# Kernel tuning notes

Hardware: AMD Instinct MI355X
Metric: run time of the kernel (lower is better)

The kernel has to match this reference:

```python
import jax, jax.numpy as jnp
import numpy as np

N_EMBD = 1024
HEAD_SIZE = 64
B, T = 8, 4096


def setup_inputs() -> dict:
    key = jax.random.key(0)
    kx, kk, kq, kv = jax.random.split(key, 4)
    scale = 1.0 / np.sqrt(N_EMBD)
    x = jax.random.normal(kx, (B, T, N_EMBD), dtype=jnp.float32)
    # nn.Linear(N_EMBD, head_size, bias=False) weights, stored as [in, out] for x @ W
    W_k = jax.random.uniform(kk, (N_EMBD, HEAD_SIZE), dtype=jnp.float32, minval=-scale, maxval=scale)
    W_q = jax.random.uniform(kq, (N_EMBD, HEAD_SIZE), dtype=jnp.float32, minval=-scale, maxval=scale)
    W_v = jax.random.uniform(kv, (N_EMBD, HEAD_SIZE), dtype=jnp.float32, minval=-scale, maxval=scale)
    return {"x": x, "W_k": W_k, "W_q": W_q, "W_v": W_v}


def reference(x, W_k, W_q, W_v) -> jnp.ndarray:
    # x: [B,T,E]; projections to [B,T,H]
    k = jnp.einsum("bte,eh->bth", x, W_k)
    q = jnp.einsum("bte,eh->bth", x, W_q)
    v = jnp.einsum("bte,eh->bth", x, W_v)
    H = W_k.shape[1]
    scores = jnp.einsum("bth,bsh->bts", q, k) * (H ** -0.5)  # [B,T,T]
    Tlen = x.shape[1]
    causal = jnp.tril(jnp.ones((Tlen, Tlen), dtype=bool))
    scores = jnp.where(causal, scores, -jnp.inf)
    attn = jax.nn.softmax(scores, axis=-1)
    # dropout is identity in eval mode (deterministic reference)
    return jnp.einsum("bts,bsh->bth", attn, v)
```

## Files before the change

### kernel.cpp

```cpp
#include <hip/hip_runtime.h>
#include <hip/hip_bf16.h>


#define BB 8
#define TT 4096
#define EE 1024
#define HH 64

typedef __attribute__((ext_vector_type(8))) short short8;
typedef __attribute__((ext_vector_type(4))) float floatx4;
typedef short8 __attribute__((may_alias)) short8_a;
typedef uint2 __attribute__((may_alias)) uint2_a;
typedef uint4 __attribute__((may_alias)) uint4_a;
typedef float4 __attribute__((may_alias)) float4_a;

#define GLDS(gp, lp)                                                     \
  __builtin_amdgcn_global_load_lds(                                      \
      (const __attribute__((address_space(1))) unsigned int*)(gp),       \
      (__attribute__((address_space(3))) unsigned int*)(lp), 16, 0, 0)

__device__ __forceinline__ unsigned short f2bf(float f) {
  union { float f; unsigned int u; } v; v.f = f;
  unsigned int r = v.u + 0x7fffu + ((v.u >> 16) & 1u);
  return (unsigned short)(r >> 16);
}
__device__ __forceinline__ unsigned int pk2(float a, float b) {
  return (unsigned int)f2bf(a) | ((unsigned int)f2bf(b) << 16);
}
__device__ __forceinline__ floatx4 fzero() {
  floatx4 z = {0.f, 0.f, 0.f, 0.f};
  return z;
}
__device__ __forceinline__ floatx4 mfma_bf16(short8 a, short8 b, floatx4 c) {
  return __builtin_amdgcn_mfma_f32_16x16x32_bf16(a, b, c, 0, 0, 0);
}
__device__ __forceinline__ short8 pack8(float4 a, float4 b) {
  union { unsigned int u[4]; short8 s; } r;
  r.u[0] = pk2(a.x, a.y);
  r.u[1] = pk2(a.z, a.w);
  r.u[2] = pk2(b.x, b.y);
  r.u[3] = pk2(b.z, b.w);
  return r.s;
}

__global__ __launch_bounds__(256) void wt_kernel(
    const float* __restrict__ Wk, const float* __restrict__ Wq,
    const float* __restrict__ Wv, unsigned short* __restrict__ wt3) {
  __shared__ float tile[64][65];
  const int m = blockIdx.y;
  const int eb = blockIdx.x;
  const float* W = (m == 0) ? Wk : ((m == 1) ? Wq : Wv);
  const int t = threadIdx.x;
  {
    const int r = t >> 2;
    const int c0 = (t & 3) * 16;
    const float* src = W + (size_t)(eb * 64 + r) * 64 + c0;
#pragma unroll
    for (int i = 0; i < 16; ++i) tile[r][c0 + i] = src[i];
  }
  __syncthreads();
  {
    const int h = t >> 2;
    const int e0 = (t & 3) * 16;
    unsigned int w[8];
#pragma unroll
    for (int i = 0; i < 8; ++i)
      w[i] = pk2(tile[e0 + 2 * i][h], tile[e0 + 2 * i + 1][h]);
    unsigned short* dst = wt3 + (size_t)(m * 64 + h) * EE + eb * 64 + e0;
    ((uint4_a*)dst)[0] = make_uint4(w[0], w[1], w[2], w[3]);
    ((uint4_a*)(dst + 8))[0] = make_uint4(w[4], w[5], w[6], w[7]);
  }
}

__global__ __launch_bounds__(256) void proj_kernel(
    const float* __restrict__ x, const unsigned short* __restrict__ wt3,
    unsigned short* __restrict__ kws, unsigned short* __restrict__ qws,
    unsigned short* __restrict__ vtws) {
  __shared__ unsigned short Bl[2][24][512];
  const int t = threadIdx.x;
  const int wv = t >> 6, lane = t & 63;
  const int l16 = lane & 15, quad = lane >> 4;
  const int mshalf = wv & 1;
  const int jbase = (wv >> 1) * 6;
  const size_t row0 = (size_t)blockIdx.x * 64;

  floatx4 acc[6][2];
#pragma unroll
  for (int j = 0; j < 6; ++j)
#pragma unroll
    for (int m2 = 0; m2 < 2; ++m2) acc[j][m2] = fzero();

  const float* xbase = x + (row0 + mshalf * 32 + l16) * EE + quad * 8;

  float4 ra[2][2][2], rb[2][2][2];
#pragma unroll
  for (int m2 = 0; m2 < 2; ++m2)
#pragma unroll
    for (int f = 0; f < 2; ++f)
#pragma unroll
      for (int g = 0; g < 2; ++g)
        ra[m2][f][g] = *(const float4_a*)(xbase + (size_t)m2 * 16 * EE + f * 32 + g * 4);

#define STAGE_B(buf, kc)                                                       \
  {                                                                            \
    _Pragma("unroll") for (int i = 0; i < 6; ++i) {                            \
      const int idx = wv * 6 + i;                                              \
      const int j = idx >> 1, f = idx & 1;                                     \
      const unsigned short* gp =                                               \
          wt3 + (size_t)(j * 16 + l16) * EE + (kc) + f * 32 + quad * 8;        \
      GLDS(gp, &Bl[buf][idx][0]);                                              \
    }                                                                          \
  }

  STAGE_B(0, 0);
  __syncthreads();

  for (int c = 0; c < 16; ++c) {
    const int cur = c & 1;
    if (c < 15) {
      STAGE_B(cur ^ 1, (c + 1) * 64);
#pragma unroll
      for (int m2 = 0; m2 < 2; ++m2)
#pragma unroll
        for (int f = 0; f < 2; ++f)
#pragma unroll
          for (int g = 0; g < 2; ++g)
            rb[m2][f][g] = *(const float4_a*)(xbase + (size_t)m2 * 16 * EE +
                                              (c + 1) * 64 + f * 32 + g * 4);
    }
    short8 af[2][2];
#pragma unroll
    for (int m2 = 0; m2 < 2; ++m2)
#pragma unroll
      for (int f = 0; f < 2; ++f) af[m2][f] = pack8(ra[m2][f][0], ra[m2][f][1]);
#pragma unroll
    for (int j = 0; j < 6; ++j)
#pragma unroll
      for (int f = 0; f < 2; ++f) {
        short8 bf = *(const short8_a*)&Bl[cur][(jbase + j) * 2 + f][lane * 8];
#pragma unroll
        for (int m2 = 0; m2 < 2; ++m2)
          acc[j][m2] = mfma_bf16(af[m2][f], bf, acc[j][m2]);
      }
#pragma unroll
    for (int m2 = 0; m2 < 2; ++m2)
#pragma unroll
      for (int f = 0; f < 2; ++f)
#pragma unroll
        for (int g = 0; g < 2; ++g) ra[m2][f][g] = rb[m2][f][g];
    __syncthreads();
  }
#undef STAGE_B

  const int b = (int)(row0 >> 12);
  const int tt0 = (int)(row0 & (TT - 1));
#pragma unroll
  for (int j = 0; j < 6; ++j) {
    const int jg = jbase + j;
    const int m = jg >> 2;
    const int h0 = (jg & 3) * 16;
#pragma unroll
    for (int m2 = 0; m2 < 2; ++m2) {
      floatx4 a = acc[j][m2];
      const int rbase = mshalf * 32 + m2 * 16 + quad * 4;
      if (m == 0) {
#pragma unroll
        for (int r = 0; r < 4; ++r)
          kws[(row0 + rbase + r) * HH + h0 + l16] = f2bf(a[r]);
      } else if (m == 1) {
#pragma unroll
        for (int r = 0; r < 4; ++r)
          qws[(row0 + rbase + r) * HH + h0 + l16] = f2bf(a[r] * 0.125f);
      } else {
        uint2 p;
        p.x = pk2(a[0], a[1]);
        p.y = pk2(a[2], a[3]);
        ((uint2_a*)&vtws[(size_t)(b * 64 + h0 + l16) * TT + tt0 + rbase])[0] = p;
      }
    }
  }
}

__global__ __launch_bounds__(256) void attn_kernel(
    const unsigned short* __restrict__ kws, const unsigned short* __restrict__ qws,
    const unsigned short* __restrict__ vtws, float* __restrict__ out) {
  __shared__ unsigned short KV[2][16][512];
  __shared__ unsigned short pb[4][16][72];
  const int t = threadIdx.x;
  const int wv = t >> 6, lane = t & 63;
  const int l16 = lane & 15, quad = lane >> 4;
  const int id = (int)blockIdx.x;
  const int r255 = id & 255;
  const int b = r255 & 7;
  const int m = r255 >> 3;
  const int jq = (id < 256) ? m : 63 - m;
  const int q0 = jq * 64;
  const int dt = jq;
  const int qrow = q0 + wv * 16 + l16;

  const unsigned short* qp = qws + ((size_t)b * TT + qrow) * HH + quad * 8;
  short8 qa0 = *(const short8_a*)(qp);
  short8 qa1 = *(const short8_a*)(qp + 32);

  floatx4 o[4];
#pragma unroll
  for (int nt = 0; nt < 4; ++nt) o[nt] = fzero();
  float lsum = 0.f;

#define STAGE_KV(buf, ks)                                                      \
  {                                                                            \
    _Pragma("unroll") for (int i = 0; i < 4; ++i) {                            \
      const int idx = wv * 4 + i;                                              \
      const unsigned short* gp;                                                \
      if (idx < 8) {                                                           \
        const int nt = idx >> 1, f = idx & 1;                                  \
        gp = kws + ((size_t)b * TT + (ks) + nt * 16 + l16) * HH + f * 32 +     \
             quad * 8;                                                         \
      } else {                                                                 \
        const int nt = (idx - 8) >> 1, f = idx & 1;                            \
        gp = vtws + ((size_t)(b * 64 + nt * 16 + l16)) * TT + (ks) + f * 32 +  \
             quad * 8;                                                         \
      }                                                                        \
      GLDS(gp, &KV[buf][idx][0]);                                              \
    }                                                                          \
  }

  STAGE_KV(0, 0);
  __syncthreads();

  for (int kt = 0; kt <= dt; ++kt) {
    const int cur = kt & 1;
    const int ks = kt * 64;
    if (kt < dt) STAGE_KV(cur ^ 1, ks + 64);

    floatx4 s[4];
#pragma unroll
    for (int nt = 0; nt < 4; ++nt) {
      short8 kf0 = *(const short8_a*)&KV[cur][nt * 2][lane * 8];
      short8 kf1 = *(const short8_a*)&KV[cur][nt * 2 + 1][lane * 8];
      floatx4 z = fzero();
      z = mfma_bf16(kf0, qa0, z);
      z = mfma_bf16(kf1, qa1, z);
      s[nt] = z;
    }
    if (kt == dt) {
#pragma unroll
      for (int nt = 0; nt < 4; ++nt)
#pragma unroll
        for (int r = 0; r < 4; ++r) {
          const int key = ks + nt * 16 + quad * 4 + r;
          if (key > qrow) s[nt][r] = -1e30f;
        }
    }
#pragma unroll
    for (int nt = 0; nt < 4; ++nt) {
      const float p0 = __expf(s[nt][0]);
      const float p1 = __expf(s[nt][1]);
      const float p2 = __expf(s[nt][2]);
      const float p3 = __expf(s[nt][3]);
      lsum += (p0 + p1) + (p2 + p3);
      uint2 pw;
      pw.x = pk2(p0, p1);
      pw.y = pk2(p2, p3);
      ((uint2_a*)&pb[wv][l16][nt * 16 + quad * 4])[0] = pw;
    }
    short8 pf0 = *(const short8_a*)&pb[wv][l16][quad * 8];
    short8 pf1 = *(const short8_a*)&pb[wv][l16][quad * 8 + 32];
#pragma unroll
    for (int nt = 0; nt < 4; ++nt) {
      short8 vf0 = *(const short8_a*)&KV[cur][8 + nt * 2][lane * 8];
      short8 vf1 = *(const short8_a*)&KV[cur][8 + nt * 2 + 1][lane * 8];
      o[nt] = mfma_bf16(vf0, pf0, o[nt]);
      o[nt] = mfma_bf16(vf1, pf1, o[nt]);
    }
    __syncthreads();
  }
#undef STAGE_KV

  float lr = lsum;
  lr += __shfl_xor(lr, 16);
  lr += __shfl_xor(lr, 32);
  const float inv = 1.0f / lr;
#pragma unroll
  for (int nt = 0; nt < 4; ++nt) {
    float4 st;
    st.x = o[nt][0] * inv;
    st.y = o[nt][1] * inv;
    st.z = o[nt][2] * inv;
    st.w = o[nt][3] * inv;
    *(float4_a*)&out[((size_t)b * TT + qrow) * HH + nt * 16 + quad * 4] = st;
  }
}

extern "C" void kernel_launch(void* const* d_in, const int* in_sizes, int n_in,
                              void* d_out, int out_size, void* d_ws, size_t ws_size,
                              hipStream_t stream) {
  const float* x = (const float*)d_in[0];
  const float* Wk = (const float*)d_in[1];
  const float* Wq = (const float*)d_in[2];
  const float* Wv = (const float*)d_in[3];
  float* out = (float*)d_out;

  unsigned short* kws = (unsigned short*)d_ws;
  unsigned short* qws = kws + (size_t)BB * TT * HH;
  unsigned short* vtws = qws + (size_t)BB * TT * HH;
  unsigned short* wt3 = vtws + (size_t)BB * TT * HH;

  hipLaunchKernelGGL(wt_kernel, dim3(16, 3), dim3(256), 0, stream, Wk, Wq, Wv, wt3);
  hipLaunchKernelGGL(proj_kernel, dim3(512), dim3(256), 0, stream, x, wt3, kws, qws,
                     vtws);
  hipLaunchKernelGGL(attn_kernel, dim3(512), dim3(256), 0, stream, kws, qws,
                     vtws, out);
}
```

Baseline: 305.0 us.

## Split long causal query tiles across key ranges with a separate combine kernel

Query tiles are split along the key dimension into 1 to 4 chunks depending on their causal length, giving 1280 blocks of roughly even work. Each block writes unnormalised partial outputs and row sums to a workspace, and a new combine kernel adds them and normalises. Two smaller changes ride along: the exponential switches to exp2 with log2(e) folded into the Q scale, and bf16 packing uses the hardware v_cvt_pk_bf16_f32 instruction. The cost is an extra launch plus partial-result traffic through global memory, and the split path is used only when the workspace is large enough.

```diff
diff --git a/kernel.cpp b/kernel.cpp
--- a/kernel.cpp
+++ b/kernel.cpp
@@ -1,11 +1,14 @@
 #include <hip/hip_runtime.h>
 #include <hip/hip_bf16.h>
+#include <math.h>
 
 
 #define BB 8
 #define TT 4096
 #define EE 1024
 #define HH 64
+#define NSLOT 160
+#define SLOTF 4160
 
 typedef __attribute__((ext_vector_type(8))) short short8;
 typedef __attribute__((ext_vector_type(4))) float floatx4;
@@ -25,7 +28,9 @@
   return (unsigned short)(r >> 16);
 }
 __device__ __forceinline__ unsigned int pk2(float a, float b) {
-  return (unsigned int)f2bf(a) | ((unsigned int)f2bf(b) << 16);
+  unsigned int r;
+  asm("v_cvt_pk_bf16_f32 %0, %1, %2" : "=v"(r) : "v"(a), "v"(b));
+  return r;
 }
 __device__ __forceinline__ floatx4 fzero() {
   floatx4 z = {0.f, 0.f, 0.f, 0.f};
@@ -170,7 +175,7 @@
       } else if (m == 1) {
 #pragma unroll
         for (int r = 0; r < 4; ++r)
-          qws[(row0 + rbase + r) * HH + h0 + l16] = f2bf(a[r] * 0.125f);
+          qws[(row0 + rbase + r) * HH + h0 + l16] = f2bf(a[r] * 0.18033688011112042f);
       } else {
         uint2 p;
         p.x = pk2(a[0], a[1]);
@@ -181,21 +186,42 @@
   }
 }
 
+template <bool SPLIT>
 __global__ __launch_bounds__(256) void attn_kernel(
     const unsigned short* __restrict__ kws, const unsigned short* __restrict__ qws,
-    const unsigned short* __restrict__ vtws, float* __restrict__ out) {
+    const unsigned short* __restrict__ vtws, float* __restrict__ dst) {
   __shared__ unsigned short KV[2][16][512];
   __shared__ unsigned short pb[4][16][72];
   const int t = threadIdx.x;
   const int wv = t >> 6, lane = t & 63;
   const int l16 = lane & 15, quad = lane >> 4;
   const int id = (int)blockIdx.x;
-  const int r255 = id & 255;
-  const int b = r255 & 7;
-  const int m = r255 >> 3;
-  const int jq = (id < 256) ? m : 63 - m;
+  int b, jq, kt0, kt1;
+  if (SPLIT) {
+    b = id & 7;
+    const int cid = id >> 3;
+    int s, S;
+    if (cid < 16) {
+      jq = cid; s = 0; S = 1;
+    } else if (cid < 48) {
+      const int u = cid - 16; jq = 16 + (u >> 1); s = u & 1; S = 2;
+    } else if (cid < 96) {
+      const int u = cid - 48; const int d = u / 3; jq = 32 + d; s = u - 3 * d; S = 3;
+    } else {
+      const int u = cid - 96; jq = 48 + (u >> 2); s = u & 3; S = 4;
+    }
+    const int n = jq + 1;
+    kt0 = (s * n) / S;
+    kt1 = ((s + 1) * n) / S;
+  } else {
+    const int r255 = id & 255;
+    b = r255 & 7;
+    const int m = r255 >> 3;
+    jq = (id < 256) ? m : 63 - m;
+    kt0 = 0;
+    kt1 = jq + 1;
+  }
   const int q0 = jq * 64;
-  const int dt = jq;
   const int qrow = q0 + wv * 16 + l16;
 
   const unsigned short* qp = qws + ((size_t)b * TT + qrow) * HH + quad * 8;
@@ -225,15 +251,15 @@
     }                                                                          \
   }
 
-  STAGE_KV(0, 0);
+  STAGE_KV(0, kt0 * 64);
   __syncthreads();
 
-  for (int kt = 0; kt <= dt; ++kt) {
-    const int cur = kt & 1;
+  for (int kt = kt0; kt < kt1; ++kt) {
+    const int cur = (kt - kt0) & 1;
     const int ks = kt * 64;
-    if (kt < dt) STAGE_KV(cur ^ 1, ks + 64);
-
-    floatx4 s[4];
+    if (kt + 1 < kt1) STAGE_KV(cur ^ 1, ks + 64);
+
+    floatx4 sc[4];
 #pragma unroll
     for (int nt = 0; nt < 4; ++nt) {
       short8 kf0 = *(const short8_a*)&KV[cur][nt * 2][lane * 8];
@@ -241,23 +267,23 @@
       floatx4 z = fzero();
       z = mfma_bf16(kf0, qa0, z);
       z = mfma_bf16(kf1, qa1, z);
-      s[nt] = z;
-    }
-    if (kt == dt) {
+      sc[nt] = z;
+    }
+    if (kt == jq) {
 #pragma unroll
       for (int nt = 0; nt < 4; ++nt)
 #pragma unroll
         for (int r = 0; r < 4; ++r) {
           const int key = ks + nt * 16 + quad * 4 + r;
-          if (key > qrow) s[nt][r] = -1e30f;
+          if (key > qrow) sc[nt][r] = -1e30f;
         }
     }
 #pragma unroll
     for (int nt = 0; nt < 4; ++nt) {
-      const float p0 = __expf(s[nt][0]);
-      const float p1 = __expf(s[nt][1]);
-      const float p2 = __expf(s[nt][2]);
-      const float p3 = __expf(s[nt][3]);
+      const float p0 = exp2f(sc[nt][0]);
+      const float p1 = exp2f(sc[nt][1]);
+      const float p2 = exp2f(sc[nt][2]);
+      const float p3 = exp2f(sc[nt][3]);
       lsum += (p0 + p1) + (p2 + p3);
       uint2 pw;
       pw.x = pk2(p0, p1);
@@ -280,15 +306,57 @@
   float lr = lsum;
   lr += __shfl_xor(lr, 16);
   lr += __shfl_xor(lr, 32);
-  const float inv = 1.0f / lr;
-#pragma unroll
-  for (int nt = 0; nt < 4; ++nt) {
-    float4 st;
-    st.x = o[nt][0] * inv;
-    st.y = o[nt][1] * inv;
-    st.z = o[nt][2] * inv;
-    st.w = o[nt][3] * inv;
-    *(float4_a*)&out[((size_t)b * TT + qrow) * HH + nt * 16 + quad * 4] = st;
+
+  if (SPLIT) {
+    float* op = dst + (size_t)id * SLOTF;
+    const int ql = wv * 16 + l16;
+#pragma unroll
+    for (int nt = 0; nt < 4; ++nt) {
+      float4 st;
+      st.x = o[nt][0];
+      st.y = o[nt][1];
+      st.z = o[nt][2];
+      st.w = o[nt][3];
+      *(float4_a*)&op[(size_t)ql * 64 + nt * 16 + quad * 4] = st;
+    }
+    if (lane < 16) op[4096 + wv * 16 + lane] = lr;
+  } else {
+    const float inv = 1.0f / lr;
+#pragma unroll
+    for (int nt = 0; nt < 4; ++nt) {
+      float4 st;
+      st.x = o[nt][0] * inv;
+      st.y = o[nt][1] * inv;
+      st.z = o[nt][2] * inv;
+      st.w = o[nt][3] * inv;
+      *(float4_a*)&dst[((size_t)b * TT + qrow) * HH + nt * 16 + quad * 4] = st;
+    }
+  }
+}
+
+__global__ __launch_bounds__(256) void comb_kernel(
+    const float* __restrict__ part, float* __restrict__ out) {
+  const int id = (int)blockIdx.x;
+  const int b = id & 7;
+  const int jq = id >> 3;
+  const int tq = jq >> 4;
+  const int S = tq + 1;
+  const int P = 8 * tq * (tq + 1) + (jq & 15) * S;
+  const int t = threadIdx.x;
+  const int r0 = t >> 6;
+  const int h = t & 63;
+  const float* s0 = part + (size_t)(b + 8 * P) * SLOTF;
+  const size_t sstr = (size_t)8 * SLOTF;
+
+#pragma unroll 4
+  for (int i = 0; i < 16; ++i) {
+    const int r = i * 4 + r0;
+    float acc = 0.f, l = 0.f;
+    for (int s2 = 0; s2 < S; ++s2) {
+      acc += s0[(size_t)s2 * sstr + (size_t)r * 64 + h];
+      l += s0[(size_t)s2 * sstr + 4096 + r];
+    }
+    out[((size_t)b * TT + jq * 64 + r) * HH + h] = acc / l;
   }
 }
 
@@ -305,10 +373,21 @@
   unsigned short* qws = kws + (size_t)BB * TT * HH;
   unsigned short* vtws = qws + (size_t)BB * TT * HH;
   unsigned short* wt3 = vtws + (size_t)BB * TT * HH;
+  float* part = (float*)(wt3 + (size_t)3 * HH * EE);
+
+  const size_t base_bytes = (size_t)3 * BB * TT * HH * 2 + (size_t)3 * HH * EE * 2;
+  const size_t need = base_bytes + (size_t)BB * NSLOT * SLOTF * 4;
+  const bool use_split = (ws_size >= need);
 
   hipLaunchKernelGGL(wt_kernel, dim3(16, 3), dim3(256), 0, stream, Wk, Wq, Wv, wt3);
   hipLaunchKernelGGL(proj_kernel, dim3(512), dim3(256), 0, stream, x, wt3, kws, qws,
                      vtws);
-  hipLaunchKernelGGL(attn_kernel, dim3(512), dim3(256), 0, stream, kws, qws,
-                     vtws, out);
-}
+  if (use_split) {
+    hipLaunchKernelGGL((attn_kernel<true>), dim3(BB * NSLOT), dim3(256), 0, stream,
+                       kws, qws, vtws, part);
+    hipLaunchKernelGGL(comb_kernel, dim3(512), dim3(256), 0, stream, part, out);
+  } else {
+    hipLaunchKernelGGL((attn_kernel<false>), dim3(512), dim3(256), 0, stream,
+                       kws, qws, vtws, out);
+  }
+}
```

After: 289.8 us. -5.0%, faster.
